# Optimization experiments

Measured on AMD Instinct MI355X. Metric: run time of the kernel, lower is better.

The kernel has to match this reference:

```python
import jax, jax.numpy as jnp
import numpy as np

N, E = 50000, 800000
NODE_DIM, EDGE_DIM = 128, 32
EGO_H, PEER_H, EDGE_H = 64, 64, 32  # node_hidden=128 split; edge_hidden=32


def setup_inputs() -> dict:
    key = jax.random.key(0)
    ks = jax.random.split(key, 9)
    x = jax.random.normal(ks[0], (N, NODE_DIM), dtype=jnp.float32)
    edge_attrs = jax.random.normal(ks[1], (E, EDGE_DIM), dtype=jnp.float32)
    edge_index = jax.random.randint(ks[2], (2, E), 0, N, dtype=jnp.int32)
    # Linear params (torch convention: W [out, in]), num_layers=1 -> single emb Linear per MLPLayer
    def lin(k, out_d, in_d):
        kw, kb = jax.random.split(k)
        s = 1.0 / np.sqrt(in_d)
        return (jax.random.uniform(kw, (out_d, in_d), minval=-s, maxval=s, dtype=jnp.float32),
                jax.random.uniform(kb, (out_d,), minval=-s, maxval=s, dtype=jnp.float32))
    W_peer, b_peer = lin(ks[3], PEER_H + EDGE_H, NODE_DIM + EDGE_DIM)
    W_ego, b_ego = lin(ks[4], EGO_H, NODE_DIM)
    W_edge, b_edge = lin(ks[5], EDGE_H, EDGE_DIM)
    return {"x": x, "edge_attrs": edge_attrs,
            "W_peer": W_peer, "b_peer": b_peer,
            "W_ego": W_ego, "b_ego": b_ego,
            "W_edge": W_edge, "b_edge": b_edge,
            "edge_index": edge_index}


def reference(x, edge_attrs, W_peer, b_peer, W_ego, b_ego, W_edge, b_edge, edge_index):
    n = x.shape[0]
    # adj_t = SparseTensor(row=ei[0], col=ei[1]).t() -> row = ei[1], col = ei[0]
    row = edge_index[1]
    col = edge_index[0]

    # ego branch
    h_ego = jax.nn.relu(x @ W_ego.T + b_ego)  # [N, EGO_H]

    # degree-based row normalization: deg^-0.5 per adj_t row, inf -> 0
    deg = jax.ops.segment_sum(jnp.ones((row.shape[0],), x.dtype), row, num_segments=n)
    dinv = jnp.where(deg > 0, jax.lax.rsqrt(jnp.maximum(deg, 1.0)) * (deg > 0), 0.0)
    dinv = jnp.where(deg > 0, deg ** -0.5, 0.0)
    norm_val = dinv[row]  # [E]

    # peer branch: gather x[row], cat edge_attrs, linear, normalize, scatter-sum over row
    peer_features = jnp.concatenate([x[row], edge_attrs], axis=1)  # [E, NODE_DIM+EDGE_DIM]
    peer_msg = norm_val[:, None] * (peer_features @ W_peer.T + b_peer)
    h_peer = jax.nn.relu(jax.ops.segment_sum(peer_msg, row, num_segments=n))  # [N, PEER_H+EDGE_H]

    # edge branch
    h_e = jax.nn.relu(edge_attrs @ W_edge.T + b_edge)  # [E, EDGE_H]
    h_e_agg = jax.ops.segment_sum(h_e, row, num_segments=n)  # adj_t.set_value(h_edge).sum(1)
    # norm.matmul(h_edge): out[i] = sum_{e: row[e]==i} norm_val[e] * h_e_agg[col[e]]
    h_e_mm = jax.ops.segment_sum(norm_val[:, None] * h_e_agg[col], row, num_segments=n)
    h_edge = jnp.concatenate([h_e_agg, h_e_mm], axis=1)  # [N, 2*EDGE_H]

    out = jnp.concatenate([h_ego, h_edge, h_peer], axis=1)  # [N, 224]
    return out
```

## Files before the change

kernel.cpp:

```cpp
#include <hip/hip_runtime.h>


typedef float f32x4 __attribute__((ext_vector_type(4)));
typedef short bf16x8 __attribute__((ext_vector_type(8)));
typedef unsigned short u16x8 __attribute__((ext_vector_type(8)));

#define BP 256

__device__ __forceinline__ unsigned short f2bf(float f) {
    unsigned u = __float_as_uint(f);
    u += 0x7fffu + ((u >> 16) & 1u);
    return (unsigned short)(u >> 16);
}
__device__ __forceinline__ float bf2f(unsigned short u) {
    return __uint_as_float((unsigned)u << 16);
}
__device__ __forceinline__ u16x8 pk8u(float4 lo, float4 hi) {
    u16x8 r;
    r[0]=f2bf(lo.x); r[1]=f2bf(lo.y); r[2]=f2bf(lo.z); r[3]=f2bf(lo.w);
    r[4]=f2bf(hi.x); r[5]=f2bf(hi.y); r[6]=f2bf(hi.z); r[7]=f2bf(hi.w);
    return r;
}
__device__ __forceinline__ bf16x8 mk_frag(ushort4 lo, ushort4 hi) {
    bf16x8 b;
    b[0]=(short)lo.x; b[1]=(short)lo.y; b[2]=(short)lo.z; b[3]=(short)lo.w;
    b[4]=(short)hi.x; b[5]=(short)hi.y; b[6]=(short)hi.z; b[7]=(short)hi.w;
    return b;
}
__device__ __forceinline__ bf16x8 ld_bfrag(const unsigned short* bp) {
    return mk_frag(*reinterpret_cast<const ushort4*>(bp),
                   *reinterpret_cast<const ushort4*>(bp + 16));
}

__global__ __launch_bounds__(256) void k_zero(int* __restrict__ deg, int N) {
    int i = blockIdx.x * blockDim.x + threadIdx.x;
    if (i < N) deg[i] = 0;
}

__global__ __launch_bounds__(256) void k_hist(const int* __restrict__ row,
                                              int* __restrict__ deg,
                                              int* __restrict__ rank, int E) {
    int e = blockIdx.x * blockDim.x + threadIdx.x;
    if (e < E) rank[e] = atomicAdd(&deg[row[e]], 1);
}

__global__ __launch_bounds__(256) void k_scan_partial(const int* __restrict__ deg,
                                                      int* __restrict__ bsum, int N) {
    __shared__ int sh[256];
    int base = blockIdx.x * 1024 + threadIdx.x * 4;
    int s = 0;
#pragma unroll
    for (int q = 0; q < 4; ++q) { int i = base + q; if (i < N) s += deg[i]; }
    sh[threadIdx.x] = s;
    __syncthreads();
    for (int off = 128; off > 0; off >>= 1) {
        if (threadIdx.x < off) sh[threadIdx.x] += sh[threadIdx.x + off];
        __syncthreads();
    }
    if (threadIdx.x == 0) bsum[blockIdx.x] = sh[0];
}

__global__ void k_scan_mid(const int* __restrict__ bsum, int* __restrict__ boff,
                           int* __restrict__ off, int NB, int N) {
    if (threadIdx.x == 0 && blockIdx.x == 0) {
        int acc = 0;
        for (int b = 0; b < NB; ++b) { boff[b] = acc; acc += bsum[b]; }
        off[N] = acc;
    }
}

__global__ __launch_bounds__(256) void k_scan_final(
    const int* __restrict__ deg, const int* __restrict__ boff,
    int* __restrict__ off,
    float* __restrict__ sd, float* __restrict__ rdeg, int* __restrict__ nstart,
    float* __restrict__ eagg, float* __restrict__ sea, int N)
{
    __shared__ int sh[256];
    int t = threadIdx.x;
    int base = blockIdx.x * 1024 + t * 4;
    int v[4];
#pragma unroll
    for (int q = 0; q < 4; ++q) v[q] = (base + q < N) ? deg[base + q] : 0;
    int ts = v[0] + v[1] + v[2] + v[3];
    sh[t] = ts;
    __syncthreads();
    int incl = ts;
    for (int d = 1; d < 256; d <<= 1) {
        int val = (t >= d) ? sh[t - d] : 0;
        __syncthreads();
        incl += val;
        sh[t] = incl;
        __syncthreads();
    }
    int running = boff[blockIdx.x] + incl - ts;
#pragma unroll
    for (int q = 0; q < 4; ++q) {
        int i = base + q;
        if (i < N) {
            int s = running, e = running + v[q];
            off[i] = s;
            int dg = v[q];
            sd[i]   = dg > 0 ? sqrtf((float)dg) : 0.f;
            rdeg[i] = dg > 0 ? 1.f / (float)dg : 0.f;
            for (int b = (s + BP - 1) / BP; b * BP < e; ++b) nstart[b] = i;
            bool zneed = (dg == 0) || ((s / BP) != ((e - 1) / BP));
            if (zneed) {
                float4 z = {0.f, 0.f, 0.f, 0.f};
                float4* pe = reinterpret_cast<float4*>(eagg + (size_t)i * 32);
                float4* ps = reinterpret_cast<float4*>(sea  + (size_t)i * 32);
#pragma unroll
                for (int q2 = 0; q2 < 8; ++q2) { pe[q2] = z; ps[q2] = z; }
            }
            running = e;
        }
    }
}

__global__ __launch_bounds__(256) void k_scatcvt(
    const float* __restrict__ ea, const int* __restrict__ row,
    const int* __restrict__ col, const int* __restrict__ off,
    const int* __restrict__ rank,
    unsigned short* __restrict__ easorted, int* __restrict__ colsort, int E)
{
    int e = blockIdx.x * blockDim.x + threadIdx.x;
    if (e >= E) return;
    int pos = off[row[e]] + rank[e];
    const float4* src = reinterpret_cast<const float4*>(ea + (size_t)e * 32);
    u16x8* dst = reinterpret_cast<u16x8*>(easorted + (size_t)pos * 32);
#pragma unroll
    for (int q = 0; q < 4; ++q)
        dst[q] = pk8u(src[2 * q], src[2 * q + 1]);
    colsort[pos] = col[e];
}

__global__ __launch_bounds__(256) void k_prepw(const float* __restrict__ W_ego,
                                               const float* __restrict__ W_peer,
                                               const float* __restrict__ W_edge,
                                               unsigned short* __restrict__ Bt,
                                               unsigned short* __restrict__ Bte) {
    int idx = blockIdx.x * blockDim.x + threadIdx.x;
    if (idx < 160 * 160) {
        int n = idx / 160, k = idx % 160;
        float v;
        if (n < 64) v = (k < 128) ? W_ego[n * 128 + k] : 0.f;
        else        v = W_peer[(n - 64) * 160 + k];
        Bt[idx] = f2bf(v);
    } else if (idx < 160 * 160 + 32 * 32) {
        int j = idx - 160 * 160;
        Bte[j] = f2bf(W_edge[j]);
    }
}

__global__ __launch_bounds__(512) void k_agg(
    const unsigned short* __restrict__ easorted,
    const int* __restrict__ off, const int* __restrict__ nstart,
    const unsigned short* __restrict__ Bte, const float* __restrict__ b_edge,
    float* __restrict__ eagg, float* __restrict__ sea, int N, int E)
{
    __shared__ unsigned short hs [BP][36];
    __shared__ unsigned short asr[BP][36];
    const int tid  = threadIdx.x;
    const int w    = tid >> 6;
    const int lane = tid & 63;
    const int n16  = lane & 15;
    const int h    = lane >> 4;
    const int P    = blockIdx.x * BP;

    {
        const int tA = w * 32 + n16;
        const int p0 = min(P + tA,      E - 1);
        const int p1 = min(P + tA + 16, E - 1);
        const unsigned short* r0 = easorted + (size_t)p0 * 32 + h * 4;
        const unsigned short* r1 = easorted + (size_t)p1 * 32 + h * 4;
        ushort4 lo0 = *reinterpret_cast<const ushort4*>(r0);
        ushort4 hi0 = *reinterpret_cast<const ushort4*>(r0 + 16);
        ushort4 lo1 = *reinterpret_cast<const ushort4*>(r1);
        ushort4 hi1 = *reinterpret_cast<const ushort4*>(r1 + 16);

        *reinterpret_cast<ushort4*>(&asr[tA][h * 4])           = lo0;
        *reinterpret_cast<ushort4*>(&asr[tA][16 + h * 4])      = hi0;
        *reinterpret_cast<ushort4*>(&asr[tA + 16][h * 4])      = lo1;
        *reinterpret_cast<ushort4*>(&asr[tA + 16][16 + h * 4]) = hi1;

        bf16x8 a0 = mk_frag(lo0, hi0);
        bf16x8 a1 = mk_frag(lo1, hi1);
        bf16x8 b0 = ld_bfrag(Bte + (size_t)n16 * 32 + h * 4);
        bf16x8 b1 = ld_bfrag(Bte + (size_t)(16 + n16) * 32 + h * 4);
        f32x4 d00 = {0.f,0.f,0.f,0.f}, d01 = {0.f,0.f,0.f,0.f};
        f32x4 d10 = {0.f,0.f,0.f,0.f}, d11 = {0.f,0.f,0.f,0.f};
        d00 = __builtin_amdgcn_mfma_f32_16x16x32_bf16(a0, b0, d00, 0, 0, 0);
        d01 = __builtin_amdgcn_mfma_f32_16x16x32_bf16(a0, b1, d01, 0, 0, 0);
        d10 = __builtin_amdgcn_mfma_f32_16x16x32_bf16(a1, b0, d10, 0, 0, 0);
        d11 = __builtin_amdgcn_mfma_f32_16x16x32_bf16(a1, b1, d11, 0, 0, 0);

        const int tr0 = w * 32 + h * 4;
        float be0 = b_edge[n16], be1 = b_edge[16 + n16];
#pragma unroll
        for (int r = 0; r < 4; ++r) {
            hs[tr0 + r][n16]           = f2bf(fmaxf(d00[r] + be0, 0.f));
            hs[tr0 + r][16 + n16]      = f2bf(fmaxf(d01[r] + be1, 0.f));
            hs[tr0 + 16 + r][n16]      = f2bf(fmaxf(d10[r] + be0, 0.f));
            hs[tr0 + 16 + r][16 + n16] = f2bf(fmaxf(d11[r] + be1, 0.f));
        }
    }
    __syncthreads();

    const int c = lane & 7, sub = lane >> 3;
    const int node0 = nstart[blockIdx.x];

    for (int n = node0 + w; n < N; n += 8) {
        int s0 = off[n];
        if (s0 >= P + BP) break;
        int e0 = off[n + 1];
        int s = max(s0, P) - P, eEnd = min(e0, P + BP) - P;
        float4 hv = {0.f,0.f,0.f,0.f}, av = {0.f,0.f,0.f,0.f};
        for (int t = s + sub; t < eEnd; t += 8) {
            ushort4 uh = *reinterpret_cast<const ushort4*>(&hs [t][c * 4]);
            ushort4 ua = *reinterpret_cast<const ushort4*>(&asr[t][c * 4]);
            hv.x += bf2f(uh.x); hv.y += bf2f(uh.y); hv.z += bf2f(uh.z); hv.w += bf2f(uh.w);
            av.x += bf2f(ua.x); av.y += bf2f(ua.y); av.z += bf2f(ua.z); av.w += bf2f(ua.w);
        }
#pragma unroll
        for (int m = 8; m < 64; m <<= 1) {
            hv.x += __shfl_xor(hv.x, m); hv.y += __shfl_xor(hv.y, m);
            hv.z += __shfl_xor(hv.z, m); hv.w += __shfl_xor(hv.w, m);
            av.x += __shfl_xor(av.x, m); av.y += __shfl_xor(av.y, m);
            av.z += __shfl_xor(av.z, m); av.w += __shfl_xor(av.w, m);
        }
        if (lane < 8) {
            float* pe = eagg + (size_t)n * 32 + c * 4;
            float* ps = sea  + (size_t)n * 32 + c * 4;
            bool interior = (s0 >= P) && (e0 <= P + BP);
            if (interior) {
                *reinterpret_cast<float4*>(pe) = hv;
                *reinterpret_cast<float4*>(ps) = av;
            } else {
                atomicAdd(pe+0,hv.x); atomicAdd(pe+1,hv.y);
                atomicAdd(pe+2,hv.z); atomicAdd(pe+3,hv.w);
                atomicAdd(ps+0,av.x); atomicAdd(ps+1,av.y);
                atomicAdd(ps+2,av.z); atomicAdd(ps+3,av.w);
            }
        }
    }
}

__global__ __launch_bounds__(256) void k_mmagg(
    const int* __restrict__ colsort, const int* __restrict__ off,
    const float* __restrict__ eagg, float* __restrict__ out, int N)
{
    int wid  = (blockIdx.x * blockDim.x + threadIdx.x) >> 6;
    int lane = threadIdx.x & 63;
    if (wid >= N) return;
    int s = off[wid], e = off[wid + 1];
    int c   = lane & 7;
    int sub = lane >> 3;
    float4 acc = {0.f, 0.f, 0.f, 0.f};
    float4 acc2 = {0.f, 0.f, 0.f, 0.f};
    for (int t0 = s; t0 < e; t0 += 16) {
        int t1 = t0 + sub, t2 = t0 + 8 + sub;
        if (t1 < e) {
            float4 v = reinterpret_cast<const float4*>(eagg + (size_t)colsort[t1] * 32)[c];
            acc.x += v.x; acc.y += v.y; acc.z += v.z; acc.w += v.w;
        }
        if (t2 < e) {
            float4 v = reinterpret_cast<const float4*>(eagg + (size_t)colsort[t2] * 32)[c];
            acc2.x += v.x; acc2.y += v.y; acc2.z += v.z; acc2.w += v.w;
        }
    }
    acc.x += acc2.x; acc.y += acc2.y; acc.z += acc2.z; acc.w += acc2.w;
#pragma unroll
    for (int m = 8; m < 64; m <<= 1) {
        acc.x += __shfl_xor(acc.x, m);
        acc.y += __shfl_xor(acc.y, m);
        acc.z += __shfl_xor(acc.z, m);
        acc.w += __shfl_xor(acc.w, m);
    }
    int dg = e - s;
    float dinv = dg > 0 ? rsqrtf((float)dg) : 0.f;
    if (lane < 8) {
        float4 o4 = {acc.x * dinv, acc.y * dinv, acc.z * dinv, acc.w * dinv};
        reinterpret_cast<float4*>(out + (size_t)wid * 224 + 96)[c] = o4;
        float4 eg = reinterpret_cast<const float4*>(eagg + (size_t)wid * 32)[c];
        reinterpret_cast<float4*>(out + (size_t)wid * 224 + 64)[c] = eg;
    }
}

__global__ __launch_bounds__(256) void k_node3(
    const float* __restrict__ x, const float* __restrict__ sea,
    const float* __restrict__ sd, const float* __restrict__ rdeg,
    const unsigned short* __restrict__ Bt,
    const float* __restrict__ b_ego, const float* __restrict__ b_peer,
    float* __restrict__ out, int N)
{
    const int lane = threadIdx.x & 63;
    const int wv   = threadIdx.x >> 6;
    const int wm   = blockIdx.x * 64 + wv * 16;
    const int n16  = lane & 15;
    const int h    = lane >> 4;

    const int m_l = min(wm + n16, N - 1);

    f32x4 acc[10];
#pragma unroll
    for (int f = 0; f < 10; ++f) acc[f] = (f32x4){0.f,0.f,0.f,0.f};

#pragma unroll
    for (int kc = 0; kc < 5; ++kc) {
        bf16x8 bfr[10];
#pragma unroll
        for (int f = 0; f < 10; ++f)
            bfr[f] = ld_bfrag(Bt + (size_t)(f * 16 + n16) * 160 + kc * 32 + h * 4);
        float4 lo, hi;
        if (kc < 4) {
            const float* ap = x + (size_t)m_l * 128 + kc * 32 + h * 4;
            lo = *reinterpret_cast<const float4*>(ap);
            hi = *reinterpret_cast<const float4*>(ap + 16);
        } else {
            float r = rdeg[m_l];
            const float* ap = sea + (size_t)m_l * 32 + h * 4;
            lo = *reinterpret_cast<const float4*>(ap);
            hi = *reinterpret_cast<const float4*>(ap + 16);
            lo.x*=r; lo.y*=r; lo.z*=r; lo.w*=r;
            hi.x*=r; hi.y*=r; hi.z*=r; hi.w*=r;
        }
        u16x8 au = pk8u(lo, hi);
        bf16x8 a;
#pragma unroll
        for (int q = 0; q < 8; ++q) a[q] = (short)au[q];
#pragma unroll
        for (int f = 0; f < 10; ++f)
            acc[f] = __builtin_amdgcn_mfma_f32_16x16x32_bf16(a, bfr[f], acc[f], 0, 0, 0);
    }

    const int r4 = h * 4;
    float sdv[4];
#pragma unroll
    for (int r = 0; r < 4; ++r) {
        int node = wm + r4 + r;
        sdv[r] = (node < N) ? sd[node] : 0.f;
    }
#pragma unroll
    for (int f = 0; f < 10; ++f) {
        int c = f * 16 + n16;
        float be = (c < 64)  ? b_ego[c] : 0.f;
        float bp = (c >= 64) ? b_peer[c - 64] : 0.f;
#pragma unroll
        for (int r = 0; r < 4; ++r) {
            int node = wm + r4 + r;
            if (node >= N) continue;
            float v = acc[f][r];
            if (c < 64)
                out[(size_t)node * 224 + c] = fmaxf(v + be, 0.f);
            else
                out[(size_t)node * 224 + 64 + c] = fmaxf(sdv[r] * (v + bp), 0.f);
        }
    }
}

extern "C" void kernel_launch(void* const* d_in, const int* in_sizes, int n_in,
                              void* d_out, int out_size, void* d_ws, size_t ws_size,
                              hipStream_t stream)
{
    const float* x      = (const float*)d_in[0];
    const float* ea     = (const float*)d_in[1];
    const float* W_peer = (const float*)d_in[2];
    const float* b_peer = (const float*)d_in[3];
    const float* W_ego  = (const float*)d_in[4];
    const float* b_ego  = (const float*)d_in[5];
    const float* W_edge = (const float*)d_in[6];
    const float* b_edge = (const float*)d_in[7];
    const int*   ei     = (const int*)d_in[8];

    const int N = in_sizes[0] / 128;
    const int E = in_sizes[8] / 2;
    const int* col = ei;
    const int* row = ei + E;
    const int nblocks = (E + BP - 1) / BP;

    int*            rank     = (int*)d_ws;
    unsigned short* easorted = (unsigned short*)(rank + E);
    int*            colsort  = (int*)(easorted + (size_t)32 * E);
    int*            deg_i    = colsort + E;
    float*          eagg     = (float*)(deg_i + N);
    float*          sea      = eagg + (size_t)32 * N;
    int*            off      = (int*)(sea + (size_t)32 * N);
    int*            bsum     = off + (N + 1);
    int*            boff     = bsum + 64;
    float*          sd       = (float*)(boff + 64);
    float*          rdeg     = sd + N;
    int*            nstart   = (int*)(rdeg + N);
    unsigned short* Bt       = (unsigned short*)(nstart + nblocks);
    unsigned short* Bte      = Bt + 160 * 160;
    float*          out      = (float*)d_out;

    const int TB = 256;
    const int NB = (N + 1023) / 1024;
    k_zero        <<<(N + TB - 1) / TB, TB, 0, stream>>>(deg_i, N);
    k_prepw       <<<(160*160 + 32*32 + TB - 1) / TB, TB, 0, stream>>>(W_ego, W_peer, W_edge, Bt, Bte);
    k_hist        <<<(E + TB - 1) / TB, TB, 0, stream>>>(row, deg_i, rank, E);
    k_scan_partial<<<NB, TB, 0, stream>>>(deg_i, bsum, N);
    k_scan_mid    <<<1, 64, 0, stream>>>(bsum, boff, off, NB, N);
    k_scan_final  <<<NB, TB, 0, stream>>>(deg_i, boff, off, sd, rdeg,
                                          nstart, eagg, sea, N);
    k_scatcvt     <<<(E + TB - 1) / TB, TB, 0, stream>>>(ea, row, col, off, rank,
                                                         easorted, colsort, E);

    k_agg<<<nblocks, 512, 0, stream>>>(easorted, off, nstart, Bte, b_edge,
                                       eagg, sea, N, E);

    const int agg_grid = (N + 3) / 4;
    k_mmagg<<<agg_grid, TB, 0, stream>>>(colsort, off, eagg, out, N);
    k_node3<<<(N + 63) / 64, TB, 0, stream>>>(x, sea, sd, rdeg, Bt,
                                              b_ego, b_peer, out, N);
}
```

Before: 202.9 us.

## Gather bf16 edge aggregates in mmagg, fuse zeroing, parallel mid-scan, nontemporal stores

Adds a kernel that converts the per-node edge aggregate to bf16 and writes the fp32 copy into the output, so the random gather in k_mmagg reads half the bytes. It also folds degree zeroing into the weight-prep kernel, replaces the serial block-offset scan with a wavefront shuffle scan, and uses nontemporal stores for the rank, sorted edge and column arrays. The bf16 gather lowers the precision of the second-hop aggregate, and the extra conversion kernel adds a launch plus a pass over the aggregate.

```diff
diff --git a/kernel.cpp b/kernel.cpp
--- a/kernel.cpp
+++ b/kernel.cpp
@@ -32,16 +32,34 @@
                    *reinterpret_cast<const ushort4*>(bp + 16));
 }
 
-__global__ __launch_bounds__(256) void k_zero(int* __restrict__ deg, int N) {
-    int i = blockIdx.x * blockDim.x + threadIdx.x;
-    if (i < N) deg[i] = 0;
+__global__ __launch_bounds__(256) void k_prepw(const float* __restrict__ W_ego,
+                                               const float* __restrict__ W_peer,
+                                               const float* __restrict__ W_edge,
+                                               unsigned short* __restrict__ Bt,
+                                               unsigned short* __restrict__ Bte,
+                                               int* __restrict__ deg, int N) {
+    int idx = blockIdx.x * blockDim.x + threadIdx.x;
+    if (idx < 160 * 160) {
+        int n = idx / 160, k = idx % 160;
+        float v;
+        if (n < 64) v = (k < 128) ? W_ego[n * 128 + k] : 0.f;
+        else        v = W_peer[(n - 64) * 160 + k];
+        Bt[idx] = f2bf(v);
+    } else if (idx < 160 * 160 + 32 * 32) {
+        int j = idx - 160 * 160;
+        Bte[j] = f2bf(W_edge[j]);
+    }
+    if (idx < N) deg[idx] = 0;
 }
 
 __global__ __launch_bounds__(256) void k_hist(const int* __restrict__ row,
                                               int* __restrict__ deg,
                                               int* __restrict__ rank, int E) {
     int e = blockIdx.x * blockDim.x + threadIdx.x;
-    if (e < E) rank[e] = atomicAdd(&deg[row[e]], 1);
+    if (e < E) {
+        int r = atomicAdd(&deg[row[e]], 1);
+        __builtin_nontemporal_store(r, &rank[e]);
+    }
 }
 
 __global__ __launch_bounds__(256) void k_scan_partial(const int* __restrict__ deg,
@@ -62,11 +80,16 @@
 
 __global__ void k_scan_mid(const int* __restrict__ bsum, int* __restrict__ boff,
                            int* __restrict__ off, int NB, int N) {
-    if (threadIdx.x == 0 && blockIdx.x == 0) {
-        int acc = 0;
-        for (int b = 0; b < NB; ++b) { boff[b] = acc; acc += bsum[b]; }
-        off[N] = acc;
-    }
+    int t = threadIdx.x;
+    int own = (t < NB) ? bsum[t] : 0;
+    int v = own;
+#pragma unroll
+    for (int d = 1; d < 64; d <<= 1) {
+        int u = __shfl_up(v, d, 64);
+        if (t >= d) v += u;
+    }
+    if (t < NB) boff[t] = v - own;
+    if (t == 63) off[N] = v;
 }
 
 __global__ __launch_bounds__(256) void k_scan_final(
@@ -129,26 +152,8 @@
     u16x8* dst = reinterpret_cast<u16x8*>(easorted + (size_t)pos * 32);
 #pragma unroll
     for (int q = 0; q < 4; ++q)
-        dst[q] = pk8u(src[2 * q], src[2 * q + 1]);
-    colsort[pos] = col[e];
-}
-
-__global__ __launch_bounds__(256) void k_prepw(const float* __restrict__ W_ego,
-                                               const float* __restrict__ W_peer,
-                                               const float* __restrict__ W_edge,
-                                               unsigned short* __restrict__ Bt,
-                                               unsigned short* __restrict__ Bte) {
-    int idx = blockIdx.x * blockDim.x + threadIdx.x;
-    if (idx < 160 * 160) {
-        int n = idx / 160, k = idx % 160;
-        float v;
-        if (n < 64) v = (k < 128) ? W_ego[n * 128 + k] : 0.f;
-        else        v = W_peer[(n - 64) * 160 + k];
-        Bt[idx] = f2bf(v);
-    } else if (idx < 160 * 160 + 32 * 32) {
-        int j = idx - 160 * 160;
-        Bte[j] = f2bf(W_edge[j]);
-    }
+        __builtin_nontemporal_store(pk8u(src[2 * q], src[2 * q + 1]), &dst[q]);
+    __builtin_nontemporal_store(col[e], &colsort[pos]);
 }
 
 __global__ __launch_bounds__(512) void k_agg(
@@ -244,9 +249,22 @@
     }
 }
 
+__global__ __launch_bounds__(256) void k_cvteagg(
+    const float* __restrict__ eagg, unsigned short* __restrict__ eagg_bf,
+    float* __restrict__ out, int N)
+{
+    int idx = blockIdx.x * blockDim.x + threadIdx.x;
+    if (idx >= N * 8) return;
+    int node = idx >> 3, c = idx & 7;
+    float4 v = reinterpret_cast<const float4*>(eagg + (size_t)node * 32)[c];
+    ushort4 u = {f2bf(v.x), f2bf(v.y), f2bf(v.z), f2bf(v.w)};
+    *reinterpret_cast<ushort4*>(eagg_bf + (size_t)node * 32 + c * 4) = u;
+    reinterpret_cast<float4*>(out + (size_t)node * 224 + 64)[c] = v;
+}
+
 __global__ __launch_bounds__(256) void k_mmagg(
     const int* __restrict__ colsort, const int* __restrict__ off,
-    const float* __restrict__ eagg, float* __restrict__ out, int N)
+    const unsigned short* __restrict__ eagg_bf, float* __restrict__ out, int N)
 {
     int wid  = (blockIdx.x * blockDim.x + threadIdx.x) >> 6;
     int lane = threadIdx.x & 63;
@@ -259,12 +277,16 @@
     for (int t0 = s; t0 < e; t0 += 16) {
         int t1 = t0 + sub, t2 = t0 + 8 + sub;
         if (t1 < e) {
-            float4 v = reinterpret_cast<const float4*>(eagg + (size_t)colsort[t1] * 32)[c];
-            acc.x += v.x; acc.y += v.y; acc.z += v.z; acc.w += v.w;
+            ushort4 u = *reinterpret_cast<const ushort4*>(
+                eagg_bf + (size_t)colsort[t1] * 32 + c * 4);
+            acc.x += bf2f(u.x); acc.y += bf2f(u.y);
+            acc.z += bf2f(u.z); acc.w += bf2f(u.w);
         }
         if (t2 < e) {
-            float4 v = reinterpret_cast<const float4*>(eagg + (size_t)colsort[t2] * 32)[c];
-            acc2.x += v.x; acc2.y += v.y; acc2.z += v.z; acc2.w += v.w;
+            ushort4 u = *reinterpret_cast<const ushort4*>(
+                eagg_bf + (size_t)colsort[t2] * 32 + c * 4);
+            acc2.x += bf2f(u.x); acc2.y += bf2f(u.y);
+            acc2.z += bf2f(u.z); acc2.w += bf2f(u.w);
         }
     }
     acc.x += acc2.x; acc.y += acc2.y; acc.z += acc2.z; acc.w += acc2.w;
@@ -280,8 +302,6 @@
     if (lane < 8) {
         float4 o4 = {acc.x * dinv, acc.y * dinv, acc.z * dinv, acc.w * dinv};
         reinterpret_cast<float4*>(out + (size_t)wid * 224 + 96)[c] = o4;
-        float4 eg = reinterpret_cast<const float4*>(eagg + (size_t)wid * 32)[c];
-        reinterpret_cast<float4*>(out + (size_t)wid * 224 + 64)[c] = eg;
     }
 }
 
@@ -377,26 +397,30 @@
     const int* row = ei + E;
     const int nblocks = (E + BP - 1) / BP;
 
-    int*            rank     = (int*)d_ws;
-    unsigned short* easorted = (unsigned short*)(rank + E);
-    int*            colsort  = (int*)(easorted + (size_t)32 * E);
-    int*            deg_i    = colsort + E;
-    float*          eagg     = (float*)(deg_i + N);
-    float*          sea      = eagg + (size_t)32 * N;
-    int*            off      = (int*)(sea + (size_t)32 * N);
-    int*            bsum     = off + (N + 1);
-    int*            boff     = bsum + 64;
-    float*          sd       = (float*)(boff + 64);
-    float*          rdeg     = sd + N;
-    int*            nstart   = (int*)(rdeg + N);
-    unsigned short* Bt       = (unsigned short*)(nstart + nblocks);
-    unsigned short* Bte      = Bt + 160 * 160;
+    char* wp = (char*)d_ws;
+    auto carve = [&](size_t bytes) { char* r = wp; wp += (bytes + 15) & ~(size_t)15; return r; };
+    int*            rank     = (int*)carve((size_t)E * 4);
+    unsigned short* easorted = (unsigned short*)carve((size_t)E * 64);
+    int*            colsort  = (int*)carve((size_t)E * 4);
+    int*            deg_i    = (int*)carve((size_t)N * 4);
+    float*          eagg     = (float*)carve((size_t)N * 128);
+    float*          sea      = (float*)carve((size_t)N * 128);
+    unsigned short* eagg_bf  = (unsigned short*)carve((size_t)N * 64);
+    int*            off      = (int*)carve((size_t)(N + 1) * 4);
+    int*            bsum     = (int*)carve(64 * 4);
+    int*            boff     = (int*)carve(64 * 4);
+    float*          sd       = (float*)carve((size_t)N * 4);
+    float*          rdeg     = (float*)carve((size_t)N * 4);
+    int*            nstart   = (int*)carve((size_t)nblocks * 4);
+    unsigned short* Bt       = (unsigned short*)carve(160 * 160 * 2);
+    unsigned short* Bte      = (unsigned short*)carve(32 * 32 * 2);
     float*          out      = (float*)d_out;
 
     const int TB = 256;
     const int NB = (N + 1023) / 1024;
-    k_zero        <<<(N + TB - 1) / TB, TB, 0, stream>>>(deg_i, N);
-    k_prepw       <<<(160*160 + 32*32 + TB - 1) / TB, TB, 0, stream>>>(W_ego, W_peer, W_edge, Bt, Bte);
+    const int prepn = max(N, 160 * 160 + 32 * 32);
+    k_prepw       <<<(prepn + TB - 1) / TB, TB, 0, stream>>>(W_ego, W_peer, W_edge,
+                                                             Bt, Bte, deg_i, N);
     k_hist        <<<(E + TB - 1) / TB, TB, 0, stream>>>(row, deg_i, rank, E);
     k_scan_partial<<<NB, TB, 0, stream>>>(deg_i, bsum, N);
     k_scan_mid    <<<1, 64, 0, stream>>>(bsum, boff, off, NB, N);
@@ -408,8 +432,10 @@
     k_agg<<<nblocks, 512, 0, stream>>>(easorted, off, nstart, Bte, b_edge,
                                        eagg, sea, N, E);
 
+    k_cvteagg<<<(N * 8 + TB - 1) / TB, TB, 0, stream>>>(eagg, eagg_bf, out, N);
+
     const int agg_grid = (N + 3) / 4;
-    k_mmagg<<<agg_grid, TB, 0, stream>>>(colsort, off, eagg, out, N);
+    k_mmagg<<<agg_grid, TB, 0, stream>>>(colsort, off, eagg_bf, out, N);
     k_node3<<<(N + 63) / 64, TB, 0, stream>>>(x, sea, sd, rdeg, Bt,
                                               b_ego, b_peer, out, N);
 }
```

Measured after the change: 248.9 us. +22.7%, slower.
